# Optimization experiments

Measured on AMD Instinct MI355X. Metric: run time of the kernel, lower is better.

Reference implementation:

```python
import jax, jax.numpy as jnp
import numpy as np

N = 256
L = 1024
ALPHA = 0.5  # GBT_alpha: bilinear transform


def _hippo_legs(n):
    # HiPPO-LegS: A[i,k] = -sqrt(2i+1)sqrt(2k+1) if i>k; -(i+1) if i==k; 0 else
    q = np.arange(n, dtype=np.float64)
    r = np.sqrt(2.0 * q + 1.0)
    A = r[:, None] * r[None, :] * (q[:, None] > q[None, :])
    A = -(A + np.diag(q + 1.0))
    B = r[:, None]  # (N, 1)
    return A.astype(np.float32), B.astype(np.float32)


def setup_inputs() -> dict:
    key = jax.random.key(0)
    k_f, = jax.random.split(key, 1)
    A_np, B_np = _hippo_legs(N)
    return {
        "f": jax.random.normal(k_f, (L, 1), dtype=jnp.float32),
        "init_state": jnp.zeros((N, 1), dtype=jnp.float32),
        "A": jnp.asarray(A_np),
        "B": jnp.asarray(B_np),
    }


def reference(f, init_state, A, B):
    n = A.shape[0]
    seq_len = f.shape[0]
    C = jnp.ones((n,), dtype=jnp.float32)  # module's self.C
    I = jnp.eye(n, dtype=jnp.float32)

    # Per-step discretization: at step i (1-indexed), step_size = 1/i.
    step_sizes = 1.0 / jnp.arange(1, seq_len + 1, dtype=jnp.float32)  # (L,)

    def discretize(ss):
        # part1 = I - ss*alpha*A ; part2 = I + ss*(1-alpha)*A
        P1 = I - ss * ALPHA * A
        P2 = I + ss * (1.0 - ALPHA) * A
        # lstsq on an invertible square system == solve
        Ad = jnp.linalg.solve(P1, P2)          # (N, N)
        Bd = ss * jnp.linalg.solve(P1, B)      # (N, 1)
        return Ad, Bd

    GBT_A, GBT_B = jax.vmap(discretize)(step_sizes)  # (L,N,N), (L,N,1)

    f_scalar = f[:, 0]  # loop uses f[i-1][0]

    def step(c_prev, inp):
        Ad, Bd, fk = inp
        c = Ad @ c_prev + Bd * fk  # (N, 1)
        y = C @ c                  # (1,)
        return c, (c, y)

    _, (c_all, y_all) = jax.lax.scan(step, init_state, (GBT_A, GBT_B, f_scalar))
    # c_all: (L, N, 1) stacked hidden states; y_all: (L, 1)
    return c_all, y_all, GBT_A, GBT_B
```

## Files before the change

kernel.cpp:

```cpp
#include <hip/hip_runtime.h>

#define LSEQ 1024
#define NDIM 256

#define O_C 0
#define O_Y (LSEQ * NDIM)
#define O_A (O_Y + LSEQ)
#define O_B (O_A + (size_t)LSEQ * NDIM * NDIM)

#define RING 128
#define GT   16
#define NGRP 68

typedef float v4f __attribute__((ext_vector_type(4)));

static __device__ __forceinline__ float frcp(float x) {
    return __builtin_amdgcn_rcpf(x);
}
static __device__ __forceinline__ float hlog2(float x) {
    return __builtin_amdgcn_logf(x);
}
static __device__ __forceinline__ float hexp2(float x) {
    return __builtin_amdgcn_exp2f(x);
}

static __device__ __forceinline__ float dpp_shr1_z(float x) {
    int r = __builtin_amdgcn_update_dpp(
        __float_as_int(x), __float_as_int(x), 0x138 , 0xF, 0xF, true);
    return __int_as_float(r);
}
static __device__ __forceinline__ float dpp_shr1_inj(float inject, float src) {
    int r = __builtin_amdgcn_update_dpp(
        __float_as_int(inject), __float_as_int(src), 0x138, 0xF, 0xF, false);
    return __int_as_float(r);
}

__global__ __launch_bounds__(256) void hippo_main(
    const float* __restrict__ f,
    const float* __restrict__ init_state,
    const float* __restrict__ Bvec,
    float* __restrict__ out)
{
    const int tid = threadIdx.x;
    const int bid = blockIdx.x;

    if (bid == 0) {
        __shared__ float c_ring[RING * NDIM];
        __shared__ float y_lds[LSEQ];
        __shared__ float f_lds[LSEQ];

        for (int i = tid; i < LSEQ; i += 256) f_lds[i] = f[i];
        __syncthreads();

        if (tid < 64) {
            const int l = tid;
            float rr[4], cc[4], baseE[4];
            #pragma unroll
            for (int e = 0; e < 4; ++e) {
                rr[e] = Bvec[4 * l + e];
                cc[e] = init_state[4 * l + e];
                baseE[e] = (float)(4 * l + 1 + e);
            }
            float T = 0.0f, S = 0.0f, ssf = 0.0f, yacc = 0.0f;
            float E = (float)(-2 * l);
            float fcur = f_lds[l];
            float fnxt = f_lds[64 + l];
            float ssfv = fcur * frcp((float)(l + 1));

#define SCAN_TICK(T_, PHASE)                                                  \
  {                                                                           \
    const int t_ = (T_);                                                      \
    float inj = __int_as_float(__builtin_amdgcn_readlane(                     \
        __float_as_int(ssfv), t_ & 63));                                      \
    T    = dpp_shr1_z(T);                                                     \
    S    = dpp_shr1_z(S);                                                     \
    yacc = dpp_shr1_z(yacc);                                                  \
    ssf  = dpp_shr1_inj(inj, ssf);                                            \
    E += 2.0f;                                                                \
    float h = frcp(E);                                                        \
    bool act = (PHASE == 1) ||                                                \
               ((PHASE == 0) ? (t_ >= l) : (t_ - l < LSEQ));                  \
    if (act) {                                                                \
      _Pragma("unroll")                                                       \
      for (int e = 0; e < 4; ++e) {                                           \
        float d    = fmaf(h, baseE[e], 1.0f);                                 \
        float invd = frcp(d);                                                 \
        float w    = fmaf(2.0f - d, cc[e], rr[e] * fmaf(-h, T, ssf));         \
        T = fmaf(rr[e], cc[e], T);                                            \
        float num = fmaf(-h * rr[e], S, w);                                   \
        float cn  = num * invd;                                               \
        S = fmaf(rr[e], cn, S);                                               \
        cc[e] = cn;                                                           \
      }                                                                       \
      yacc += (cc[0] + cc[1]) + (cc[2] + cc[3]);                              \
      v4f cv = { cc[0], cc[1], cc[2], cc[3] };                                \
      *reinterpret_cast<v4f*>(&c_ring[(t_ & (RING - 1)) * NDIM + 4 * l]) = cv;\
      if (l == 63) y_lds[t_ - 63] = yacc;                                     \
    }                                                                         \
  }

            int grp = 0;
            for (; grp < 4; ++grp) {
                const int tb = grp * GT;
                #pragma unroll
                for (int g = 0; g < GT; ++g) SCAN_TICK(tb + g, 0);
                __syncthreads();
            }
            for (; grp < 64; ++grp) {
                const int tb = grp * GT;
                if ((tb & 63) == 0) {
                    fcur = fnxt;
                    int idx = tb + 64 + l;
                    fnxt = f_lds[(idx < LSEQ) ? idx : 0];
                    ssfv = fcur * frcp((float)(tb + l + 1));
                }
                #pragma unroll
                for (int g = 0; g < GT; ++g) SCAN_TICK(tb + g, 1);
                __syncthreads();
            }
            for (; grp < NGRP; ++grp) {
                const int tb = grp * GT;
                #pragma unroll
                for (int g = 0; g < GT; ++g) SCAN_TICK(tb + g, 2);
                __syncthreads();
            }
            __syncthreads();
#undef SCAN_TICK
        } else {
            const int wv = tid >> 6;
            const int lane = tid & 63;
            for (int grp = 0; grp <= NGRP; ++grp) {
                const int r0 = grp * GT - 80;
                const int lo = (wv == 1) ? 0 : (wv == 2) ? 6 : 11;
                const int hi = (wv == 1) ? 5 : (wv == 2) ? 10 : 15;
                for (int ri = lo; ri <= hi; ++ri) {
                    int r = r0 + ri;
                    if (r >= 0 && r < LSEQ) {
                        int slot = (r + lane) & (RING - 1);
                        v4f dv = *reinterpret_cast<const v4f*>(
                            &c_ring[slot * NDIM + 4 * lane]);
                        __builtin_nontemporal_store(dv,
                            reinterpret_cast<v4f*>(
                                out + O_C + (size_t)r * NDIM + 4 * lane));
                    }
                }
                if (wv == 3 && lane < GT) {
                    int r = r0 + lane;
                    if (r >= 0 && r < LSEQ)
                        __builtin_nontemporal_store(y_lds[r], out + O_Y + r);
                }
                __syncthreads();
            }
        }
    } else {
        const int k = bid - 1;
        const int lane = tid & 63;
        const int wave = tid >> 6;
        const float kp = (float)(k + 1);
        const float ss = 1.0f / kp;
        const float h  = 0.5f * ss;

        __shared__ float s_cc[NDIM], s_rowco[NDIM], s_diag[NDIM], s_Lp[NDIM];
        __shared__ int   s_NZp[NDIM];
        __shared__ float s_wL[4];
        __shared__ int   s_wNZ[4];

        const int i = tid;
        const float r    = Bvec[i];
        const float dd   = fmaf(h, (float)(i + 1), 1.0f);
        const float invd = 1.0f / dd;
        const float g    = (1.0f - h * (float)i) * invd;

        const int zer = (g == 0.0f) ? 1 : 0;
        const int neg = (g < 0.0f) ? 1 : 0;
        float sL = zer ? 0.0f : hlog2(fabsf(g));
        int   sNZ = neg | (zer << 16);

        #pragma unroll
        for (int off = 1; off < 64; off <<= 1) {
            float tL  = __shfl_up(sL, off);
            int   tNZ = __shfl_up(sNZ, off);
            if (lane >= off) { sL += tL; sNZ += tNZ; }
        }
        if (lane == 63) { s_wL[wave] = sL; s_wNZ[wave] = sNZ; }
        __syncthreads();
        for (int ww = 0; ww < wave; ++ww) { sL += s_wL[ww]; sNZ += s_wNZ[ww]; }

        s_Lp[i]    = sL;
        s_NZp[i]   = sNZ;
        s_cc[i]    = r * invd;
        s_rowco[i] = -2.0f * h * r * invd;
        s_diag[i]  = fmaf(2.0f, invd, -1.0f);
        __syncthreads();

        {
            float P;
            if (i == 0) P = 1.0f;
            else {
                float Lw = s_Lp[i - 1]; int nzw = s_NZp[i - 1];
                P = (nzw >> 16) ? 0.0f : hexp2(Lw);
                if (nzw & 1) P = -P;
            }
            out[O_B + (size_t)k * NDIM + i] = -s_rowco[i] * P;
        }

        float Lj[4], ccj[4]; int NZj[4];
        #pragma unroll
        for (int e = 0; e < 4; ++e) {
            int j = 4 * lane + e;
            Lj[e]  = s_Lp[j];
            NZj[e] = s_NZp[j];
            ccj[e] = s_cc[j];
        }

        const int i0 = wave * 64;
        float* outA = out + O_A + (size_t)k * (NDIM * NDIM) + 4 * lane;
        #pragma unroll 4
        for (int ir = 0; ir < 64; ++ir) {
            const int irow = i0 + ir;
            const int ip = (irow > 0) ? (irow - 1) : 0;
            const float Lpi = s_Lp[ip];
            const int   NZi = s_NZp[ip];
            const float rc  = s_rowco[irow];
            const float dg  = s_diag[irow];
            float v[4];
            #pragma unroll
            for (int e = 0; e < 4; ++e) {
                const int j = 4 * lane + e;
                float wv = hexp2(Lpi - Lj[e]);
                int nzd = NZi - NZj[e];
                wv = (nzd >> 16) ? 0.0f : wv;
                wv = (nzd & 1) ? -wv : wv;
                float val = rc * ccj[e] * wv;
                v[e] = (j < irow) ? val : ((j == irow) ? dg : 0.0f);
            }
            v4f vv = { v[0], v[1], v[2], v[3] };
            __builtin_nontemporal_store(
                vv, reinterpret_cast<v4f*>(outA + (size_t)irow * NDIM));
        }
    }
}

extern "C" void kernel_launch(void* const* d_in, const int* in_sizes, int n_in,
                              void* d_out, int out_size, void* d_ws, size_t ws_size,
                              hipStream_t stream) {
    (void)in_sizes; (void)n_in; (void)d_ws; (void)ws_size; (void)out_size;
    const float* f    = (const float*)d_in[0];
    const float* init = (const float*)d_in[1];
    const float* Bv   = (const float*)d_in[3];
    float* outp       = (float*)d_out;
    hippo_main<<<1 + LSEQ, 256, 0, stream>>>(f, init, Bv, outp);
}
```

Baseline: 383.6 us.

## Replace block barriers with LDS progress flags between scan and writer waves

The scan wave and the three writer waves in block 0 now coordinate through shared-memory progress counters instead of __syncthreads after every 16-step group. The scan wave publishes how far it has got and checks backpressure against the slowest writer so the ring buffer is not overrun. Writers spin-wait on that counter and each handles every third row on its own. This removes lockstep barrier stalls on the serial critical path, at the cost of spin-polling, reliance on LDS memory ordering, and y being written by every lane rather than one.

```diff
diff --git a/kernel.cpp b/kernel.cpp
--- a/kernel.cpp
+++ b/kernel.cpp
@@ -10,7 +10,6 @@
 
 #define RING 128
 #define GT   16
-#define NGRP 68
 
 typedef float v4f __attribute__((ext_vector_type(4)));
 
@@ -48,7 +47,11 @@
         __shared__ float c_ring[RING * NDIM];
         __shared__ float y_lds[LSEQ];
         __shared__ float f_lds[LSEQ];
-
+        __shared__ int   s_prog;
+        __shared__ int   s_fprog[3];
+
+        if (tid == 0) s_prog = 0;
+        if (tid < 3)  s_fprog[tid] = tid;
         for (int i = tid; i < LSEQ; i += 256) f_lds[i] = f[i];
         __syncthreads();
 
@@ -67,11 +70,26 @@
             float fnxt = f_lds[64 + l];
             float ssfv = fcur * frcp((float)(l + 1));
 
-#define SCAN_TICK(T_, PHASE)                                                  \
+#define PUBLISH(V)                                                            \
+  { asm volatile("s_waitcnt lgkmcnt(0)" ::: "memory");                        \
+    *(volatile int*)&s_prog = (V); }
+
+#define BACKPRESSURE(TB)                                                      \
+  { const int need = (TB) - 112;                                              \
+    for (;;) {                                                                \
+      int m0 = *(volatile int*)&s_fprog[0];                                   \
+      int m1 = *(volatile int*)&s_fprog[1];                                   \
+      int m2 = *(volatile int*)&s_fprog[2];                                   \
+      int mm = m0 < m1 ? m0 : m1; mm = mm < m2 ? mm : m2;                     \
+      if (mm >= need) break;                                                  \
+      __builtin_amdgcn_s_sleep(1);                                            \
+    } }
+
+#define SCAN_TICK(T_, RL_, PHASE)                                             \
   {                                                                           \
     const int t_ = (T_);                                                      \
     float inj = __int_as_float(__builtin_amdgcn_readlane(                     \
-        __float_as_int(ssfv), t_ & 63));                                      \
+        __float_as_int(ssfv), (RL_)));                                        \
     T    = dpp_shr1_z(T);                                                     \
     S    = dpp_shr1_z(S);                                                     \
     yacc = dpp_shr1_z(yacc);                                                  \
@@ -95,61 +113,57 @@
       yacc += (cc[0] + cc[1]) + (cc[2] + cc[3]);                              \
       v4f cv = { cc[0], cc[1], cc[2], cc[3] };                                \
       *reinterpret_cast<v4f*>(&c_ring[(t_ & (RING - 1)) * NDIM + 4 * l]) = cv;\
-      if (l == 63) y_lds[t_ - 63] = yacc;                                     \
+      y_lds[t_ - l] = yacc;     \
     }                                                                         \
   }
 
-            int grp = 0;
-            for (; grp < 4; ++grp) {
-                const int tb = grp * GT;
+            int tb = 0;
+            for (int q = 0; q < 4; ++q) {
                 #pragma unroll
-                for (int g = 0; g < GT; ++g) SCAN_TICK(tb + g, 0);
-                __syncthreads();
-            }
-            for (; grp < 64; ++grp) {
-                const int tb = grp * GT;
-                if ((tb & 63) == 0) {
-                    fcur = fnxt;
-                    int idx = tb + 64 + l;
-                    fnxt = f_lds[(idx < LSEQ) ? idx : 0];
-                    ssfv = fcur * frcp((float)(tb + l + 1));
+                for (int g = 0; g < GT; ++g) SCAN_TICK(tb + g, q * GT + g, 0);
+                PUBLISH(tb + GT);
+                tb += GT;
+            }
+            for (int ch = 1; ch < 16; ++ch) {
+                fcur = fnxt;
+                int idx = ch * 64 + 64 + l;
+                fnxt = f_lds[(idx < LSEQ) ? idx : 0];
+                ssfv = fcur * frcp((float)(ch * 64 + l + 1));
+                for (int q = 0; q < 4; ++q) {
+                    BACKPRESSURE(tb);
+                    #pragma unroll
+                    for (int g = 0; g < GT; ++g) SCAN_TICK(tb + g, q * GT + g, 1);
+                    PUBLISH(tb + GT);
+                    tb += GT;
                 }
+            }
+            for (int q = 0; q < 4; ++q) {
+                BACKPRESSURE(tb);
                 #pragma unroll
-                for (int g = 0; g < GT; ++g) SCAN_TICK(tb + g, 1);
-                __syncthreads();
-            }
-            for (; grp < NGRP; ++grp) {
-                const int tb = grp * GT;
-                #pragma unroll
-                for (int g = 0; g < GT; ++g) SCAN_TICK(tb + g, 2);
-                __syncthreads();
-            }
-            __syncthreads();
+                for (int g = 0; g < GT; ++g) SCAN_TICK(tb + g, q * GT + g, 2);
+                PUBLISH(tb + GT);
+                tb += GT;
+            }
 #undef SCAN_TICK
+#undef PUBLISH
+#undef BACKPRESSURE
         } else {
-            const int wv = tid >> 6;
+            const int wv   = tid >> 6;
             const int lane = tid & 63;
-            for (int grp = 0; grp <= NGRP; ++grp) {
-                const int r0 = grp * GT - 80;
-                const int lo = (wv == 1) ? 0 : (wv == 2) ? 6 : 11;
-                const int hi = (wv == 1) ? 5 : (wv == 2) ? 10 : 15;
-                for (int ri = lo; ri <= hi; ++ri) {
-                    int r = r0 + ri;
-                    if (r >= 0 && r < LSEQ) {
-                        int slot = (r + lane) & (RING - 1);
-                        v4f dv = *reinterpret_cast<const v4f*>(
-                            &c_ring[slot * NDIM + 4 * lane]);
-                        __builtin_nontemporal_store(dv,
-                            reinterpret_cast<v4f*>(
-                                out + O_C + (size_t)r * NDIM + 4 * lane));
-                    }
-                }
-                if (wv == 3 && lane < GT) {
-                    int r = r0 + lane;
-                    if (r >= 0 && r < LSEQ)
-                        __builtin_nontemporal_store(y_lds[r], out + O_Y + r);
-                }
-                __syncthreads();
+            for (int r = wv - 1; r < LSEQ; r += 3) {
+                while (*(volatile int*)&s_prog < r + 64)
+                    __builtin_amdgcn_s_sleep(1);
+                int slot = (r + lane) & (RING - 1);
+                v4f dv = *reinterpret_cast<const v4f*>(
+                    &c_ring[slot * NDIM + 4 * lane]);
+                float yv = y_lds[r];
+                __builtin_nontemporal_store(dv,
+                    reinterpret_cast<v4f*>(
+                        out + O_C + (size_t)r * NDIM + 4 * lane));
+                if (lane == 0)
+                    __builtin_nontemporal_store(yv, out + O_Y + r);
+                asm volatile("" ::: "memory");
+                *(volatile int*)&s_fprog[wv - 1] = r + 3;
             }
         }
     } else {
```

Result: no change. 383.3 us (-0.1%).

## Split serial scan across two wavefronts with LDS flag handoff instead of block barriers

Applied to the files above, without the earlier changes.

The sequential state scan in block 0 is split across two wavefronts, each owning 128 state components (2 per lane), with the boundary values (T, S, ssf, y) passed from the first to the second through an LDS ring. Block-wide __syncthreads are replaced by spin-wait flags (GATE/PUBLISH) between the producer waves and two dedicated writer waves. The intent is to halve the per-tick serial work on the critical path and stop the scan stalling on the writers at every group. The cost is spin-polling overhead, an added pipeline lag for the second wave, and reliance on LDS ordering through volatile accesses and waitcnt.

```diff
diff --git a/kernel.cpp b/kernel.cpp
--- a/kernel.cpp
+++ b/kernel.cpp
@@ -10,9 +10,9 @@
 
 #define RING 128
 #define GT   16
-#define NGRP 68
 
 typedef float v4f __attribute__((ext_vector_type(4)));
+typedef float v2f __attribute__((ext_vector_type(2)));
 
 static __device__ __forceinline__ float frcp(float x) {
     return __builtin_amdgcn_rcpf(x);
@@ -34,6 +34,17 @@
         __float_as_int(inject), __float_as_int(src), 0x138, 0xF, 0xF, false);
     return __int_as_float(r);
 }
+
+#define GATE(VAR, NEED)                                                      \
+  { const int need_ = (NEED);                                                \
+    for (int sp_ = 0; sp_ < (1 << 22); ++sp_) {                              \
+      if (*(volatile int*)&(VAR) >= need_) break;                            \
+      __builtin_amdgcn_s_sleep(1);                                           \
+    } }
+
+#define PUBLISH(VAR, V)                                                      \
+  { asm volatile("s_waitcnt lgkmcnt(0)" ::: "memory");                       \
+    *(volatile int*)&(VAR) = (V); }
 
 __global__ __launch_bounds__(256) void hippo_main(
     const float* __restrict__ f,
@@ -46,110 +57,180 @@
 
     if (bid == 0) {
         __shared__ float c_ring[RING * NDIM];
+        __shared__ float f_lds[LSEQ];
         __shared__ float y_lds[LSEQ];
-        __shared__ float f_lds[LSEQ];
-
+        __shared__ v4f   b_ring[RING];
+        __shared__ int   s_p0, s_p1, s_f0, s_f1;
+
+        const int wv = tid >> 6;
+        const int l  = tid & 63;
+
+        if (tid == 0) { s_p0 = 0; s_p1 = 0; s_f0 = 0; s_f1 = 0; }
         for (int i = tid; i < LSEQ; i += 256) f_lds[i] = f[i];
         __syncthreads();
 
-        if (tid < 64) {
-            const int l = tid;
-            float rr[4], cc[4], baseE[4];
-            #pragma unroll
-            for (int e = 0; e < 4; ++e) {
-                rr[e] = Bvec[4 * l + e];
-                cc[e] = init_state[4 * l + e];
-                baseE[e] = (float)(4 * l + 1 + e);
-            }
-            float T = 0.0f, S = 0.0f, ssf = 0.0f, yacc = 0.0f;
+        if (wv == 0) {
+            float rr0 = Bvec[2 * l],     rr1 = Bvec[2 * l + 1];
+            float c0  = init_state[2*l], c1  = init_state[2*l + 1];
+            const float bE0 = (float)(2 * l + 1), bE1 = (float)(2 * l + 2);
+            float T = 0.f, S = 0.f, ssf = 0.f, ya = 0.f;
             float E = (float)(-2 * l);
-            float fcur = f_lds[l];
-            float fnxt = f_lds[64 + l];
+            float fcur = f_lds[l], fnxt = f_lds[64 + l];
             float ssfv = fcur * frcp((float)(l + 1));
 
-#define SCAN_TICK(T_, PHASE)                                                  \
-  {                                                                           \
-    const int t_ = (T_);                                                      \
+#define TICK_A(T_, ACT)                                                       \
+  { const int t_ = (T_);                                                      \
     float inj = __int_as_float(__builtin_amdgcn_readlane(                     \
         __float_as_int(ssfv), t_ & 63));                                      \
-    T    = dpp_shr1_z(T);                                                     \
-    S    = dpp_shr1_z(S);                                                     \
-    yacc = dpp_shr1_z(yacc);                                                  \
-    ssf  = dpp_shr1_inj(inj, ssf);                                            \
-    E += 2.0f;                                                                \
-    float h = frcp(E);                                                        \
-    bool act = (PHASE == 1) ||                                                \
-               ((PHASE == 0) ? (t_ >= l) : (t_ - l < LSEQ));                  \
-    if (act) {                                                                \
-      _Pragma("unroll")                                                       \
-      for (int e = 0; e < 4; ++e) {                                           \
-        float d    = fmaf(h, baseE[e], 1.0f);                                 \
-        float invd = frcp(d);                                                 \
-        float w    = fmaf(2.0f - d, cc[e], rr[e] * fmaf(-h, T, ssf));         \
-        T = fmaf(rr[e], cc[e], T);                                            \
-        float num = fmaf(-h * rr[e], S, w);                                   \
-        float cn  = num * invd;                                               \
-        S = fmaf(rr[e], cn, S);                                               \
-        cc[e] = cn;                                                           \
-      }                                                                       \
-      yacc += (cc[0] + cc[1]) + (cc[2] + cc[3]);                              \
-      v4f cv = { cc[0], cc[1], cc[2], cc[3] };                                \
-      *reinterpret_cast<v4f*>(&c_ring[(t_ & (RING - 1)) * NDIM + 4 * l]) = cv;\
-      if (l == 63) y_lds[t_ - 63] = yacc;                                     \
-    }                                                                         \
-  }
-
-            int grp = 0;
-            for (; grp < 4; ++grp) {
-                const int tb = grp * GT;
-                #pragma unroll
-                for (int g = 0; g < GT; ++g) SCAN_TICK(tb + g, 0);
-                __syncthreads();
-            }
-            for (; grp < 64; ++grp) {
-                const int tb = grp * GT;
+    T = dpp_shr1_z(T); S = dpp_shr1_z(S); ya = dpp_shr1_z(ya);                \
+    ssf = dpp_shr1_inj(inj, ssf);                                             \
+    E += 2.0f; float h = frcp(E);                                             \
+    if (ACT) {                                                                \
+      float d0 = fmaf(h, bE0, 1.0f); float i0 = frcp(d0);                     \
+      float w0 = fmaf(2.0f - d0, c0, rr0 * fmaf(-h, T, ssf));                 \
+      T = fmaf(rr0, c0, T);                                                   \
+      float n0 = fmaf(-h * rr0, S, w0); c0 = n0 * i0;                         \
+      S = fmaf(rr0, c0, S);                                                   \
+      float d1 = fmaf(h, bE1, 1.0f); float i1 = frcp(d1);                     \
+      float w1 = fmaf(2.0f - d1, c1, rr1 * fmaf(-h, T, ssf));                 \
+      T = fmaf(rr1, c1, T);                                                   \
+      float n1 = fmaf(-h * rr1, S, w1); c1 = n1 * i1;                         \
+      S = fmaf(rr1, c1, S);                                                   \
+      ya += (c0 + c1);                                                        \
+      v2f cv = { c0, c1 };                                                    \
+      *reinterpret_cast<v2f*>(&c_ring[(t_ & 127) * NDIM + 2 * l]) = cv;       \
+      if (l == 63) { v4f bw = { T, S, ssf, ya };                              \
+                     b_ring[t_ & 127] = bw; }                                 \
+    } }
+
+            int tb = 0;
+            for (int grp = 0; grp < 4; ++grp, tb += GT) {
+                #pragma unroll
+                for (int g = 0; g < GT; ++g) TICK_A(tb + g, (tb + g) >= l);
+                PUBLISH(s_p0, tb + GT);
+            }
+            for (int grp = 4; grp < 64; ++grp, tb += GT) {
                 if ((tb & 63) == 0) {
                     fcur = fnxt;
                     int idx = tb + 64 + l;
                     fnxt = f_lds[(idx < LSEQ) ? idx : 0];
                     ssfv = fcur * frcp((float)(tb + l + 1));
                 }
-                #pragma unroll
-                for (int g = 0; g < GT; ++g) SCAN_TICK(tb + g, 1);
-                __syncthreads();
-            }
-            for (; grp < NGRP; ++grp) {
-                const int tb = grp * GT;
-                #pragma unroll
-                for (int g = 0; g < GT; ++g) SCAN_TICK(tb + g, 2);
-                __syncthreads();
-            }
-            __syncthreads();
-#undef SCAN_TICK
+                if (tb >= 128) GATE(s_f0, tb - 112);
+                if (tb >= 176) GATE(s_p1, tb - 175);
+                #pragma unroll
+                for (int g = 0; g < GT; ++g) TICK_A(tb + g, true);
+                PUBLISH(s_p0, tb + GT);
+            }
+            for (int grp = 64; grp < 68; ++grp, tb += GT) {
+                GATE(s_f0, tb - 112);
+                GATE(s_p1, tb - 175);
+                #pragma unroll
+                for (int g = 0; g < GT; ++g) TICK_A(tb + g, (tb + g) - l < LSEQ);
+                PUBLISH(s_p0, tb + GT);
+            }
+#undef TICK_A
+        } else if (wv == 1) {
+            float rr0 = Bvec[128 + 2 * l],     rr1 = Bvec[128 + 2 * l + 1];
+            float c0  = init_state[128 + 2*l], c1  = init_state[128 + 2*l + 1];
+            const float bE0 = (float)(128 + 2 * l + 1);
+            const float bE1 = (float)(128 + 2 * l + 2);
+            float T = 0.f, S = 0.f, ssf = 0.f, ya = 0.f;
+            float E = (float)(-2 * l);
+            const bool l0 = (l == 0);
+
+#define TICK_B(T_, G_, ACT)                                                   \
+  { const int t_ = (T_);                                                      \
+    T = dpp_shr1_z(T); S = dpp_shr1_z(S); ya = dpp_shr1_z(ya);                \
+    ssf = dpp_shr1_z(ssf);                                                    \
+    { v4f bb = bbuf[G_];                                                      \
+      if (l0) { T = bb.x; S = bb.y; ssf = bb.z; ya = bb.w; } }                \
+    E += 2.0f; float h = frcp(E);                                             \
+    if (ACT) {                                                                \
+      float d0 = fmaf(h, bE0, 1.0f); float i0 = frcp(d0);                     \
+      float w0 = fmaf(2.0f - d0, c0, rr0 * fmaf(-h, T, ssf));                 \
+      T = fmaf(rr0, c0, T);                                                   \
+      float n0 = fmaf(-h * rr0, S, w0); c0 = n0 * i0;                         \
+      S = fmaf(rr0, c0, S);                                                   \
+      float d1 = fmaf(h, bE1, 1.0f); float i1 = frcp(d1);                     \
+      float w1 = fmaf(2.0f - d1, c1, rr1 * fmaf(-h, T, ssf));                 \
+      T = fmaf(rr1, c1, T);                                                   \
+      float n1 = fmaf(-h * rr1, S, w1); c1 = n1 * i1;                         \
+      S = fmaf(rr1, c1, S);                                                   \
+      ya += (c0 + c1);                                                        \
+      v2f cv = { c0, c1 };                                                    \
+      *reinterpret_cast<v2f*>(&c_ring[(t_ & 127) * NDIM + 128 + 2 * l]) = cv; \
+      y_lds[t_ - l] = ya;                                                     \
+    } }
+
+#define PREFETCH_B(TB)                                                        \
+    v4f bbuf[GT];                                                             \
+    _Pragma("unroll")                                                         \
+    for (int g = 0; g < GT; ++g)                                              \
+        bbuf[g] = b_ring[((TB) + 63 + g) & 127];
+
+            int tb = 0;
+            for (int grp = 0; grp < 4; ++grp, tb += GT) {
+                GATE(s_p0, tb + 79);
+                PREFETCH_B(tb);
+                #pragma unroll
+                for (int g = 0; g < GT; ++g) TICK_B(tb + g, g, (tb + g) >= l);
+                PUBLISH(s_p1, tb + GT);
+            }
+            for (int grp = 4; grp < 64; ++grp, tb += GT) {
+                GATE(s_p0, tb + 79);
+                if (tb >= 128) GATE(s_f1, tb - 112);
+                PREFETCH_B(tb);
+                #pragma unroll
+                for (int g = 0; g < GT; ++g) TICK_B(tb + g, g, true);
+                PUBLISH(s_p1, tb + GT);
+            }
+            for (int grp = 64; grp < 68; ++grp, tb += GT) {
+                { int need = tb + 79; if (need > 1088) need = 1088;
+                  GATE(s_p0, need); }
+                GATE(s_f1, tb - 112);
+                PREFETCH_B(tb);
+                #pragma unroll
+                for (int g = 0; g < GT; ++g) TICK_B(tb + g, g, (tb + g) - l < LSEQ);
+                PUBLISH(s_p1, tb + GT);
+            }
+#undef TICK_B
+#undef PREFETCH_B
+        } else if (wv == 2) {
+            for (int r = 0; r < LSEQ; r += GT) {
+                GATE(s_p0, r + 79);
+                #pragma unroll
+                for (int q = 0; q < GT; ++q) {
+                    int rw = r + q;
+                    int slot = (rw + l) & 127;
+                    v2f dv = *reinterpret_cast<const v2f*>(
+                        &c_ring[slot * NDIM + 2 * l]);
+                    __builtin_nontemporal_store(dv,
+                        reinterpret_cast<v2f*>(
+                            out + O_C + (size_t)rw * NDIM + 2 * l));
+                }
+                asm volatile("s_waitcnt lgkmcnt(0)" ::: "memory");
+                *(volatile int*)&s_f0 = r + GT;
+            }
         } else {
-            const int wv = tid >> 6;
-            const int lane = tid & 63;
-            for (int grp = 0; grp <= NGRP; ++grp) {
-                const int r0 = grp * GT - 80;
-                const int lo = (wv == 1) ? 0 : (wv == 2) ? 6 : 11;
-                const int hi = (wv == 1) ? 5 : (wv == 2) ? 10 : 15;
-                for (int ri = lo; ri <= hi; ++ri) {
-                    int r = r0 + ri;
-                    if (r >= 0 && r < LSEQ) {
-                        int slot = (r + lane) & (RING - 1);
-                        v4f dv = *reinterpret_cast<const v4f*>(
-                            &c_ring[slot * NDIM + 4 * lane]);
-                        __builtin_nontemporal_store(dv,
-                            reinterpret_cast<v4f*>(
-                                out + O_C + (size_t)r * NDIM + 4 * lane));
-                    }
+            for (int r = 0; r < LSEQ; r += GT) {
+                GATE(s_p1, r + 79);
+                #pragma unroll
+                for (int q = 0; q < GT; ++q) {
+                    int rw = r + q;
+                    int slot = (rw + l) & 127;
+                    v2f dv = *reinterpret_cast<const v2f*>(
+                        &c_ring[slot * NDIM + 128 + 2 * l]);
+                    __builtin_nontemporal_store(dv,
+                        reinterpret_cast<v2f*>(
+                            out + O_C + (size_t)rw * NDIM + 128 + 2 * l));
                 }
-                if (wv == 3 && lane < GT) {
-                    int r = r0 + lane;
-                    if (r >= 0 && r < LSEQ)
-                        __builtin_nontemporal_store(y_lds[r], out + O_Y + r);
+                if (l < GT) {
+                    float yv = y_lds[r + l];
+                    __builtin_nontemporal_store(yv, out + O_Y + r + l);
                 }
-                __syncthreads();
+                asm volatile("s_waitcnt lgkmcnt(0)" ::: "memory");
+                *(volatile int*)&s_f1 = r + GT;
             }
         }
     } else {
@@ -227,11 +308,11 @@
             #pragma unroll
             for (int e = 0; e < 4; ++e) {
                 const int j = 4 * lane + e;
-                float wv = hexp2(Lpi - Lj[e]);
+                float wvv = hexp2(Lpi - Lj[e]);
                 int nzd = NZi - NZj[e];
-                wv = (nzd >> 16) ? 0.0f : wv;
-                wv = (nzd & 1) ? -wv : wv;
-                float val = rc * ccj[e] * wv;
+                wvv = (nzd >> 16) ? 0.0f : wvv;
+                wvv = (nzd & 1) ? -wvv : wvv;
+                float val = rc * ccj[e] * wvv;
                 v[e] = (j < irow) ? val : ((j == irow) ? dg : 0.0f);
             }
             v4f vv = { v[0], v[1], v[2], v[3] };
```

Measured after the change: 366.7 us. 4.4% less time.
